# Kernel tuning notes

Measured on AMD Instinct MI355X. Metric: run time of the kernel, lower is better.

## Reference

```python
import jax, jax.numpy as jnp
import numpy as np

TAU = 1.0        # gumbel-softmax temperature
H = 8            # n_heads
RD = 32          # routing_dim


def setup_inputs() -> dict:
    key = jax.random.key(0)
    k1, k2, k3, k4, k5 = jax.random.split(key, 5)
    B, T, C = 2, 2048, 1024
    x = jax.random.normal(k1, (B, T, C), dtype=jnp.float32)
    # base adjacency [H,T,T]; keep diagonal free so each causal row has a finite logit
    base_mask = jax.random.randint(k2, (H, T, T), 0, 2).astype(bool)
    base_mask = base_mask & ~jnp.eye(T, dtype=bool)[None]
    # pre-sampled standard Gumbel noise (matches F.gumbel_softmax internals)
    u = jax.random.uniform(k3, (B, H, T, T), dtype=jnp.float32, minval=1e-9, maxval=1.0)
    gumbel = -jnp.log(-jnp.log(u))
    scale = 1.0 / np.sqrt(C).astype(np.float32)
    Wq = jax.random.normal(k4, (C, H * RD), dtype=jnp.float32) * scale
    Wk = jax.random.normal(k5, (C, H * RD), dtype=jnp.float32) * scale
    return {"x": x, "base_mask": base_mask, "gumbel": gumbel, "Wq": Wq, "Wk": Wk}


def reference(x, base_mask, gumbel, Wq, Wk):
    B, T, C = x.shape
    # routing projections -> [B,T,H,RD]
    sq = (x @ Wq).reshape(B, T, H, RD)
    sk = (x @ Wk).reshape(B, T, H, RD)
    # pairwise edge scores [B,H,T,T]
    scores = jnp.einsum("bihd,bjhd->bhij", sq, sk) / np.sqrt(RD).astype(np.float32)
    # causal mask (j > i) OR already-connected base edges -> -inf
    causal = jnp.triu(jnp.ones((T, T), dtype=bool), 1)
    mask = causal[None, None] | base_mask[None]
    scores = jnp.where(mask, -jnp.inf, scores)
    # gumbel-softmax (training path, hard=False): softmax((logits + g) / tau)
    return jax.nn.softmax((scores + gumbel) / TAU, axis=-1)
```

## Files before the change

kernel.cpp:

```cpp
#include <hip/hip_runtime.h>
#include <hip/hip_bf16.h>
#include <math.h>

#define TT    2048
#define HH    8
#define RDIM  32
#define BB    2

typedef float  f4  __attribute__((ext_vector_type(4)));
typedef int    i4  __attribute__((ext_vector_type(4)));
typedef uint   u2  __attribute__((ext_vector_type(2)));
typedef uint   u4  __attribute__((ext_vector_type(4)));
typedef short  s8v __attribute__((ext_vector_type(8)));

__device__ __forceinline__ uint rnd16(float x) {
    return (__float_as_uint(x) + 0x8000u) >> 16;
}

union v8cast { u4 u; s8v s; };

__global__ __launch_bounds__(256) void wt_prep(
    const float* __restrict__ Wq,
    const float* __restrict__ Wk,
    ushort* __restrict__ Wt)
{
    __shared__ float T[64][68];
    const int k0 = blockIdx.x * 64;
    const int n0 = blockIdx.y * 64;
    const float* W = (n0 < 256) ? Wq : Wk;
    const int nloc = n0 & 255;
    const int tid = threadIdx.x;

    #pragma unroll
    for (int r = 0; r < 4; ++r) {
        int kl  = (tid >> 4) + r * 16;
        int nl4 = (tid & 15) * 4;
        f4 v = *(const f4*)&W[(size_t)(k0 + kl) * 256 + nloc + nl4];
        T[nl4 + 0][kl] = v.x;
        T[nl4 + 1][kl] = v.y;
        T[nl4 + 2][kl] = v.z;
        T[nl4 + 3][kl] = v.w;
    }
    __syncthreads();

    const int nl = tid >> 2;
    const int kq = (tid & 3) * 16;
    u4 o0, o1;
    #pragma unroll
    for (int j = 0; j < 4; ++j) {
        uint lo = rnd16(T[nl][kq + 2 * j]);
        uint hi = rnd16(T[nl][kq + 2 * j + 1]);
        ((uint*)&o0)[j] = (hi << 16) | lo;
    }
    #pragma unroll
    for (int j = 0; j < 4; ++j) {
        uint lo = rnd16(T[nl][kq + 8 + 2 * j]);
        uint hi = rnd16(T[nl][kq + 8 + 2 * j + 1]);
        ((uint*)&o1)[j] = (hi << 16) | lo;
    }
    ushort* dst = Wt + (size_t)(n0 + nl) * 1024 + k0 + kq;
    *(u4*)dst = o0;
    *(u4*)(dst + 8) = o1;
}

__global__ __launch_bounds__(256) void proj_mfma(
    const float* __restrict__ x,
    const ushort* __restrict__ Wt,
    ushort* __restrict__ sqb,
    ushort* __restrict__ skb)
{
    const int tid = threadIdx.x;
    const int l   = tid & 63;
    const int w   = __builtin_amdgcn_readfirstlane(tid) >> 6;
    const int cl  = l & 15;
    const int g4  = l >> 4;
    const int m0  = (blockIdx.x * 4 + w) * 16;
    const int n0  = blockIdx.y * 64;

    f4 acc0 = {0,0,0,0}, acc1 = {0,0,0,0}, acc2 = {0,0,0,0}, acc3 = {0,0,0,0};

    const float*  xrow = x + (size_t)(m0 + cl) * 1024;
    const ushort* wbase = Wt + (size_t)(n0 + cl) * 1024;

    for (int ks = 0; ks < 32; ++ks) {
        const int k = ks * 32 + g4 * 8;
        f4 xa = *(const f4*)&xrow[k];
        f4 xb2 = *(const f4*)&xrow[k + 4];
        v8cast bf;
        ((uint*)&bf.u)[0] = (rnd16(xa.y) << 16) | rnd16(xa.x);
        ((uint*)&bf.u)[1] = (rnd16(xa.w) << 16) | rnd16(xa.z);
        ((uint*)&bf.u)[2] = (rnd16(xb2.y) << 16) | rnd16(xb2.x);
        ((uint*)&bf.u)[3] = (rnd16(xb2.w) << 16) | rnd16(xb2.z);
        s8v a0 = *(const s8v*)(wbase + 0 * 16 * 1024 + k);
        s8v a1 = *(const s8v*)(wbase + 1 * 16 * 1024 + k);
        s8v a2 = *(const s8v*)(wbase + 2 * 16 * 1024 + k);
        s8v a3 = *(const s8v*)(wbase + 3 * 16 * 1024 + k);
        acc0 = __builtin_amdgcn_mfma_f32_16x16x32_bf16(a0, bf.s, acc0, 0, 0, 0);
        acc1 = __builtin_amdgcn_mfma_f32_16x16x32_bf16(a1, bf.s, acc1, 0, 0, 0);
        acc2 = __builtin_amdgcn_mfma_f32_16x16x32_bf16(a2, bf.s, acc2, 0, 0, 0);
        acc3 = __builtin_amdgcn_mfma_f32_16x16x32_bf16(a3, bf.s, acc3, 0, 0, 0);
    }

    const int m = m0 + cl;
    const int nbase = n0 + g4 * 4;
    ushort* obase = (n0 < 256) ? (sqb + (size_t)m * 256 + nbase)
                               : (skb + (size_t)m * 256 + (nbase - 256));
    f4 accs[4] = {acc0, acc1, acc2, acc3};
    #pragma unroll
    for (int t = 0; t < 4; ++t) {
        u2 pk;
        pk.x = (rnd16(accs[t][1]) << 16) | rnd16(accs[t][0]);
        pk.y = (rnd16(accs[t][3]) << 16) | rnd16(accs[t][2]);
        *(u2*)(obase + t * 16) = pk;
    }
}

__global__ __launch_bounds__(512) void score_mfma(
    const ushort* __restrict__ sqb,
    const ushort* __restrict__ skb,
    const float*  __restrict__ gumbel,
    const int*    __restrict__ mask,
    float* __restrict__ out)
{
    const int tid = threadIdx.x;
    const int l   = tid & 63;
    const int w   = __builtin_amdgcn_readfirstlane(tid) >> 6;
    const int bh  = blockIdx.x & 15;
    const int sp  = blockIdx.x >> 4;
    const int h   = bh & (HH - 1);
    const int b   = bh >> 3;
    const int cl  = l & 15;
    const int g4  = l >> 4;
    const float RS = 0.17677669529663687f;

    __shared__ float sums_lds[8][16];

    const ushort* sqbase = sqb + ((size_t)b * TT) * 256 + h * RDIM + g4 * 8;
    const ushort* skbase = skb + ((size_t)b * TT) * 256 + h * RDIM + g4 * 8;
    const float*  gb = gumbel + (size_t)bh * TT * TT;
    const int*    mb = mask + (size_t)h * TT * TT;
    float*        ob = out + (size_t)bh * TT * TT;

    #pragma unroll 1
    for (int half = 0; half < 2; ++half) {
        const int s      = half ? (127 - sp) : sp;
        const int i0     = s * 16;
        const int ntiles = s + 1;
        const int zstart = ntiles * 16;
        const int i      = i0 + cl;

        s8v bfrag = *(const s8v*)(sqbase + (size_t)i * 256);

        const float* grow = gb + (size_t)i * TT;
        const int*   mrow = mb + (size_t)i * TT;
        float*       orow = ob + (size_t)i * TT;

        float sum = 0.f;
        u2 p[8][2];
        #pragma unroll
        for (int it = 0; it < 8; ++it) {
            const int jt0 = 2 * w + it * 16;
            #pragma unroll
            for (int u = 0; u < 2; ++u) {
                const int jt = jt0 + u;
                if (jt < ntiles) {
                    s8v afrag = *(const s8v*)(skbase + (size_t)(jt * 16 + cl) * 256);
                    f4 z = {0.f, 0.f, 0.f, 0.f};
                    f4 c = __builtin_amdgcn_mfma_f32_16x16x32_bf16(
                               afrag, bfrag, z, 0, 0, 0);
                    const int jb = jt * 16 + g4 * 4;
                    f4 gv = *(const f4*)&grow[jb];
                    i4 mv = *(const i4*)&mrow[jb];
                    float e0 = (jb + 0 > i || mv.x) ? 0.f : __expf(fmaf(c[0], RS, gv.x));
                    float e1 = (jb + 1 > i || mv.y) ? 0.f : __expf(fmaf(c[1], RS, gv.y));
                    float e2 = (jb + 2 > i || mv.z) ? 0.f : __expf(fmaf(c[2], RS, gv.z));
                    float e3 = (jb + 3 > i || mv.w) ? 0.f : __expf(fmaf(c[3], RS, gv.w));
                    sum += (e0 + e1) + (e2 + e3);
                    p[it][u].x = (rnd16(e1) << 16) | rnd16(e0);
                    p[it][u].y = (rnd16(e3) << 16) | rnd16(e2);
                }
            }
        }

        sum += __shfl_xor(sum, 16);
        sum += __shfl_xor(sum, 32);
        if (l < 16) sums_lds[w][l] = sum;
        __syncthreads();
        float t = 0.f;
        #pragma unroll
        for (int ww = 0; ww < 8; ++ww) t += sums_lds[ww][cl];
        const float rinv = 1.0f / t;
        __syncthreads();

        #pragma unroll
        for (int it = 0; it < 8; ++it) {
            const int jt0 = 2 * w + it * 16;
            #pragma unroll
            for (int u = 0; u < 2; ++u) {
                const int jt = jt0 + u;
                if (jt < ntiles) {
                    const int jb = jt * 16 + g4 * 4;
                    f4 v;
                    v.x = __uint_as_float(p[it][u].x << 16) * rinv;
                    v.y = __uint_as_float(p[it][u].x & 0xffff0000u) * rinv;
                    v.z = __uint_as_float(p[it][u].y << 16) * rinv;
                    v.w = __uint_as_float(p[it][u].y & 0xffff0000u) * rinv;
                    *(f4*)&orow[jb] = v;
                }
            }
        }

        for (int r = 0; r < 16; ++r) {
            for (int cz = zstart + tid * 4; cz < TT; cz += 512 * 4) {
                f4 zz = {0.f, 0.f, 0.f, 0.f};
                *(f4*)&ob[(size_t)(i0 + r) * TT + cz] = zz;
            }
        }
    }
}

extern "C" void kernel_launch(void* const* d_in, const int* in_sizes, int n_in,
                              void* d_out, int out_size, void* d_ws, size_t ws_size,
                              hipStream_t stream) {
    const float* x      = (const float*)d_in[0];
    const int*   bmask  = (const int*)d_in[1];
    const float* gumbel = (const float*)d_in[2];
    const float* Wq     = (const float*)d_in[3];
    const float* Wk     = (const float*)d_in[4];
    float* out = (float*)d_out;

    ushort* sqb = (ushort*)d_ws;
    ushort* skb = sqb + (size_t)4096 * 256;
    ushort* Wt  = skb + (size_t)4096 * 256;

    wt_prep<<<dim3(16, 8), 256, 0, stream>>>(Wq, Wk, Wt);

    proj_mfma<<<dim3(64, 8), 256, 0, stream>>>(x, Wt, sqb, skb);

    score_mfma<<<1024, 512, 0, stream>>>(sqb, skb, gumbel, bmask, out);
}
```

Measured before the change: 187.8 us.

## Double-buffer score kernel loads, stage probabilities in LDS, use nontemporal gumbel/zero stores

Software-pipelines the score kernel: the K fragment, gumbel and mask loads for the next iteration are issued before the current MFMA/exp work. The packed bf16 probabilities move from a register array into a 64 KB LDS buffer, and launch bounds now request 2 blocks per CU to cut register pressure. Gumbel reads and the zero-fill stores use nontemporal hints to avoid cache pollution. The added LDS footprint may cap occupancy, and the prefetch buffers add registers.

```diff
diff --git a/kernel.cpp b/kernel.cpp
--- a/kernel.cpp
+++ b/kernel.cpp
@@ -115,7 +115,7 @@
     }
 }
 
-__global__ __launch_bounds__(512) void score_mfma(
+__global__ __launch_bounds__(512, 2) void score_mfma(
     const ushort* __restrict__ sqb,
     const ushort* __restrict__ skb,
     const float*  __restrict__ gumbel,
@@ -133,6 +133,7 @@
     const int g4  = l >> 4;
     const float RS = 0.17677669529663687f;
 
+    __shared__ u2    p_lds[8][16][64];
     __shared__ float sums_lds[8][16];
 
     const ushort* sqbase = sqb + ((size_t)b * TT) * 256 + h * RDIM + g4 * 8;
@@ -155,32 +156,55 @@
         const int*   mrow = mb + (size_t)i * TT;
         float*       orow = ob + (size_t)i * TT;
 
+        s8v af[2][2];
+        f4  gv[2][2];
+        i4  mv[2][2];
+
+        #define PLOAD(buf_, it_) do {                                          \
+            _Pragma("unroll")                                                  \
+            for (int u_ = 0; u_ < 2; ++u_) {                                   \
+                const int jt_ = 2 * w + (it_) * 16 + u_;                       \
+                if (jt_ < ntiles) {                                            \
+                    af[buf_][u_] = *(const s8v*)(skbase +                      \
+                                     (size_t)(jt_ * 16 + cl) * 256);           \
+                    const int jb_ = jt_ * 16 + g4 * 4;                         \
+                    gv[buf_][u_] = __builtin_nontemporal_load(                 \
+                                     (const f4*)&grow[jb_]);                   \
+                    mv[buf_][u_] = *(const i4*)&mrow[jb_];                     \
+                }                                                              \
+            }                                                                  \
+        } while (0)
+
+        PLOAD(0, 0);
+
         float sum = 0.f;
-        u2 p[8][2];
         #pragma unroll
         for (int it = 0; it < 8; ++it) {
-            const int jt0 = 2 * w + it * 16;
+            const int pb = it & 1;
+            if (it < 7) PLOAD(pb ^ 1, it + 1);
             #pragma unroll
             for (int u = 0; u < 2; ++u) {
-                const int jt = jt0 + u;
+                const int jt = 2 * w + it * 16 + u;
                 if (jt < ntiles) {
-                    s8v afrag = *(const s8v*)(skbase + (size_t)(jt * 16 + cl) * 256);
                     f4 z = {0.f, 0.f, 0.f, 0.f};
                     f4 c = __builtin_amdgcn_mfma_f32_16x16x32_bf16(
-                               afrag, bfrag, z, 0, 0, 0);
+                               af[pb][u], bfrag, z, 0, 0, 0);
                     const int jb = jt * 16 + g4 * 4;
-                    f4 gv = *(const f4*)&grow[jb];
-                    i4 mv = *(const i4*)&mrow[jb];
-                    float e0 = (jb + 0 > i || mv.x) ? 0.f : __expf(fmaf(c[0], RS, gv.x));
-                    float e1 = (jb + 1 > i || mv.y) ? 0.f : __expf(fmaf(c[1], RS, gv.y));
-                    float e2 = (jb + 2 > i || mv.z) ? 0.f : __expf(fmaf(c[2], RS, gv.z));
-                    float e3 = (jb + 3 > i || mv.w) ? 0.f : __expf(fmaf(c[3], RS, gv.w));
+                    f4 gvv = gv[pb][u];
+                    i4 mvv = mv[pb][u];
+                    float e0 = (jb + 0 > i || mvv.x) ? 0.f : __expf(fmaf(c[0], RS, gvv.x));
+                    float e1 = (jb + 1 > i || mvv.y) ? 0.f : __expf(fmaf(c[1], RS, gvv.y));
+                    float e2 = (jb + 2 > i || mvv.z) ? 0.f : __expf(fmaf(c[2], RS, gvv.z));
+                    float e3 = (jb + 3 > i || mvv.w) ? 0.f : __expf(fmaf(c[3], RS, gvv.w));
                     sum += (e0 + e1) + (e2 + e3);
-                    p[it][u].x = (rnd16(e1) << 16) | rnd16(e0);
-                    p[it][u].y = (rnd16(e3) << 16) | rnd16(e2);
+                    u2 pk;
+                    pk.x = (rnd16(e1) << 16) | rnd16(e0);
+                    pk.y = (rnd16(e3) << 16) | rnd16(e2);
+                    p_lds[w][it * 2 + u][l] = pk;
                 }
             }
         }
+        #undef PLOAD
 
         sum += __shfl_xor(sum, 16);
         sum += __shfl_xor(sum, 32);
@@ -193,27 +217,24 @@
         __syncthreads();
 
         #pragma unroll
-        for (int it = 0; it < 8; ++it) {
-            const int jt0 = 2 * w + it * 16;
-            #pragma unroll
-            for (int u = 0; u < 2; ++u) {
-                const int jt = jt0 + u;
-                if (jt < ntiles) {
-                    const int jb = jt * 16 + g4 * 4;
-                    f4 v;
-                    v.x = __uint_as_float(p[it][u].x << 16) * rinv;
-                    v.y = __uint_as_float(p[it][u].x & 0xffff0000u) * rinv;
-                    v.z = __uint_as_float(p[it][u].y << 16) * rinv;
-                    v.w = __uint_as_float(p[it][u].y & 0xffff0000u) * rinv;
-                    *(f4*)&orow[jb] = v;
-                }
+        for (int sx = 0; sx < 16; ++sx) {
+            const int jt = 2 * w + (sx >> 1) * 16 + (sx & 1);
+            if (jt < ntiles) {
+                const int jb = jt * 16 + g4 * 4;
+                u2 pk = p_lds[w][sx][l];
+                f4 v;
+                v.x = __uint_as_float(pk.x << 16) * rinv;
+                v.y = __uint_as_float(pk.x & 0xffff0000u) * rinv;
+                v.z = __uint_as_float(pk.y << 16) * rinv;
+                v.w = __uint_as_float(pk.y & 0xffff0000u) * rinv;
+                *(f4*)&orow[jb] = v;
             }
         }
 
         for (int r = 0; r < 16; ++r) {
             for (int cz = zstart + tid * 4; cz < TT; cz += 512 * 4) {
                 f4 zz = {0.f, 0.f, 0.f, 0.f};
-                *(f4*)&ob[(size_t)(i0 + r) * TT + cz] = zz;
+                __builtin_nontemporal_store(zz, (f4*)&ob[(size_t)(i0 + r) * TT + cz]);
             }
         }
     }
@@ -234,7 +255,6 @@
     ushort* Wt  = skb + (size_t)4096 * 256;
 
     wt_prep<<<dim3(16, 8), 256, 0, stream>>>(Wq, Wk, Wt);
-
     proj_mfma<<<dim3(64, 8), 256, 0, stream>>>(x, Wt, sqb, skb);
 
     score_mfma<<<1024, 512, 0, stream>>>(sqb, skb, gumbel, bmask, out);
```

New measurement: 197.6 us, median of 3. 5.2% more time.

## Software-pipeline score kernel loads and stage probabilities in LDS across halves

Applied to the files above, without the earlier changes.

Restructures the score kernel into a 3-deep register pipeline that issues key fragment, gumbel and mask loads two groups ahead of the MFMA/exp compute. The packed bf16 probabilities move from registers to LDS so more waves can stay resident, and launch bounds request 2 blocks per CU. The second half's first loads are issued before the first half's normalise/write pass so that latency is hidden. The zero fill also switches to nontemporal stores. It adds 64KB of LDS per block and double-buffers the reduction sums, which may limit occupancy.

```diff
diff --git a/kernel.cpp b/kernel.cpp
--- a/kernel.cpp
+++ b/kernel.cpp
@@ -115,7 +115,7 @@
     }
 }
 
-__global__ __launch_bounds__(512) void score_mfma(
+__global__ __launch_bounds__(512, 2) void score_mfma(
     const ushort* __restrict__ sqb,
     const ushort* __restrict__ skb,
     const float*  __restrict__ gumbel,
@@ -133,7 +133,8 @@
     const int g4  = l >> 4;
     const float RS = 0.17677669529663687f;
 
-    __shared__ float sums_lds[8][16];
+    __shared__ u2    p_lds[8][16][64];
+    __shared__ float sums_lds[2][8][16];
 
     const ushort* sqbase = sqb + ((size_t)b * TT) * 256 + h * RDIM + g4 * 8;
     const ushort* skbase = skb + ((size_t)b * TT) * 256 + h * RDIM + g4 * 8;
@@ -141,82 +142,151 @@
     const int*    mb = mask + (size_t)h * TT * TT;
     float*        ob = out + (size_t)bh * TT * TT;
 
-    #pragma unroll 1
-    for (int half = 0; half < 2; ++half) {
-        const int s      = half ? (127 - sp) : sp;
-        const int i0     = s * 16;
-        const int ntiles = s + 1;
-        const int zstart = ntiles * 16;
-        const int i      = i0 + cl;
-
-        s8v bfrag = *(const s8v*)(sqbase + (size_t)i * 256);
-
-        const float* grow = gb + (size_t)i * TT;
-        const int*   mrow = mb + (size_t)i * TT;
-        float*       orow = ob + (size_t)i * TT;
-
-        float sum = 0.f;
-        u2 p[8][2];
-        #pragma unroll
-        for (int it = 0; it < 8; ++it) {
-            const int jt0 = 2 * w + it * 16;
-            #pragma unroll
-            for (int u = 0; u < 2; ++u) {
-                const int jt = jt0 + u;
-                if (jt < ntiles) {
-                    s8v afrag = *(const s8v*)(skbase + (size_t)(jt * 16 + cl) * 256);
-                    f4 z = {0.f, 0.f, 0.f, 0.f};
-                    f4 c = __builtin_amdgcn_mfma_f32_16x16x32_bf16(
-                               afrag, bfrag, z, 0, 0, 0);
-                    const int jb = jt * 16 + g4 * 4;
-                    f4 gv = *(const f4*)&grow[jb];
-                    i4 mv = *(const i4*)&mrow[jb];
-                    float e0 = (jb + 0 > i || mv.x) ? 0.f : __expf(fmaf(c[0], RS, gv.x));
-                    float e1 = (jb + 1 > i || mv.y) ? 0.f : __expf(fmaf(c[1], RS, gv.y));
-                    float e2 = (jb + 2 > i || mv.z) ? 0.f : __expf(fmaf(c[2], RS, gv.z));
-                    float e3 = (jb + 3 > i || mv.w) ? 0.f : __expf(fmaf(c[3], RS, gv.w));
-                    sum += (e0 + e1) + (e2 + e3);
-                    p[it][u].x = (rnd16(e1) << 16) | rnd16(e0);
-                    p[it][u].y = (rnd16(e3) << 16) | rnd16(e2);
-                }
-            }
-        }
-
-        sum += __shfl_xor(sum, 16);
-        sum += __shfl_xor(sum, 32);
-        if (l < 16) sums_lds[w][l] = sum;
-        __syncthreads();
-        float t = 0.f;
-        #pragma unroll
-        for (int ww = 0; ww < 8; ++ww) t += sums_lds[ww][cl];
-        const float rinv = 1.0f / t;
-        __syncthreads();
-
-        #pragma unroll
-        for (int it = 0; it < 8; ++it) {
-            const int jt0 = 2 * w + it * 16;
-            #pragma unroll
-            for (int u = 0; u < 2; ++u) {
-                const int jt = jt0 + u;
-                if (jt < ntiles) {
-                    const int jb = jt * 16 + g4 * 4;
-                    f4 v;
-                    v.x = __uint_as_float(p[it][u].x << 16) * rinv;
-                    v.y = __uint_as_float(p[it][u].x & 0xffff0000u) * rinv;
-                    v.z = __uint_as_float(p[it][u].y << 16) * rinv;
-                    v.w = __uint_as_float(p[it][u].y & 0xffff0000u) * rinv;
-                    *(f4*)&orow[jb] = v;
-                }
-            }
-        }
-
-        for (int r = 0; r < 16; ++r) {
-            for (int cz = zstart + tid * 4; cz < TT; cz += 512 * 4) {
-                f4 zz = {0.f, 0.f, 0.f, 0.f};
-                *(f4*)&ob[(size_t)(i0 + r) * TT + cz] = zz;
-            }
-        }
-    }
+    const int s0_ = sp,        s1_ = 127 - sp;
+    const int i00 = s0_ * 16,  i01 = s1_ * 16;
+    const int nt0 = s0_ + 1,   nt1 = s1_ + 1;
+    const int i_0 = i00 + cl,  i_1 = i01 + cl;
+    const float* grow0 = gb + (size_t)i_0 * TT;
+    const float* grow1 = gb + (size_t)i_1 * TT;
+    const int*   mrow0 = mb + (size_t)i_0 * TT;
+    const int*   mrow1 = mb + (size_t)i_1 * TT;
+    float*       orow0 = ob + (size_t)i_0 * TT;
+    float*       orow1 = ob + (size_t)i_1 * TT;
+
+    s8v bf0 = *(const s8v*)(sqbase + (size_t)i_0 * 256);
+    s8v bf1 = *(const s8v*)(sqbase + (size_t)i_1 * 256);
+
+    s8v af[3][2];
+    f4  gv[3][2];
+    i4  mv[3][2];
+
+    #define PLOAD(gp_) do {                                                   \
+        const int buf_ = (gp_) % 3;                                           \
+        const int pr_  = (gp_) & 7;                                           \
+        const bool hh_ = (gp_) >= 8;                                          \
+        const int nt_  = hh_ ? nt1 : nt0;                                     \
+        const float* g_ = hh_ ? grow1 : grow0;                                \
+        const int*   m_ = hh_ ? mrow1 : mrow0;                                \
+        _Pragma("unroll")                                                     \
+        for (int u_ = 0; u_ < 2; ++u_) {                                      \
+            const int jt_ = 2 * w + pr_ * 16 + u_;                            \
+            if (jt_ < nt_) {                                                  \
+                af[buf_][u_] = *(const s8v*)(skbase +                         \
+                                 (size_t)(jt_ * 16 + cl) * 256);              \
+                const int jb_ = jt_ * 16 + g4 * 4;                            \
+                gv[buf_][u_] = *(const f4*)&g_[jb_];                          \
+                mv[buf_][u_] = *(const i4*)&m_[jb_];                          \
+            }                                                                 \
+        }                                                                     \
+    } while (0)
+
+    #define PCOMPUTE(gp_, sum_) do {                                          \
+        const int buf_ = (gp_) % 3;                                           \
+        const int pr_  = (gp_) & 7;                                           \
+        const bool hh_ = (gp_) >= 8;                                          \
+        const int nt_  = hh_ ? nt1 : nt0;                                     \
+        const int iw_  = hh_ ? i_1 : i_0;                                     \
+        const s8v bfr_ = hh_ ? bf1 : bf0;                                     \
+        _Pragma("unroll")                                                     \
+        for (int u_ = 0; u_ < 2; ++u_) {                                      \
+            const int jt_ = 2 * w + pr_ * 16 + u_;                            \
+            if (jt_ < nt_) {                                                  \
+                f4 z_ = {0.f, 0.f, 0.f, 0.f};                                 \
+                f4 c_ = __builtin_amdgcn_mfma_f32_16x16x32_bf16(              \
+                            af[buf_][u_], bfr_, z_, 0, 0, 0);                 \
+                const int jb_ = jt_ * 16 + g4 * 4;                            \
+                f4 gvv_ = gv[buf_][u_];                                       \
+                i4 mvv_ = mv[buf_][u_];                                       \
+                float e0_ = (jb_ + 0 > iw_ || mvv_.x) ? 0.f : __expf(fmaf(c_[0], RS, gvv_.x)); \
+                float e1_ = (jb_ + 1 > iw_ || mvv_.y) ? 0.f : __expf(fmaf(c_[1], RS, gvv_.y)); \
+                float e2_ = (jb_ + 2 > iw_ || mvv_.z) ? 0.f : __expf(fmaf(c_[2], RS, gvv_.z)); \
+                float e3_ = (jb_ + 3 > iw_ || mvv_.w) ? 0.f : __expf(fmaf(c_[3], RS, gvv_.w)); \
+                sum_ += (e0_ + e1_) + (e2_ + e3_);                            \
+                u2 pk_;                                                       \
+                pk_.x = (rnd16(e1_) << 16) | rnd16(e0_);                      \
+                pk_.y = (rnd16(e3_) << 16) | rnd16(e2_);                      \
+                p_lds[w][pr_ * 2 + u_][l] = pk_;                              \
+            }                                                                 \
+        }                                                                     \
+    } while (0)
+
+    #define REDUCE(hbuf_, sum_, rinv_) do {                                   \
+        float v_ = sum_;                                                      \
+        v_ += __shfl_xor(v_, 16);                                             \
+        v_ += __shfl_xor(v_, 32);                                             \
+        if (l < 16) sums_lds[hbuf_][w][l] = v_;                               \
+        __syncthreads();                                                      \
+        float t_ = 0.f;                                                       \
+        _Pragma("unroll")                                                     \
+        for (int ww_ = 0; ww_ < 8; ++ww_) t_ += sums_lds[hbuf_][ww_][cl];     \
+        rinv_ = 1.0f / t_;                                                    \
+    } while (0)
+
+    #define PASS2(rinv_, nt_, orow_) do {                                     \
+        _Pragma("unroll")                                                     \
+        for (int sx_ = 0; sx_ < 16; ++sx_) {                                  \
+            const int jt_ = 2 * w + (sx_ >> 1) * 16 + (sx_ & 1);              \
+            if (jt_ < nt_) {                                                  \
+                const int jb_ = jt_ * 16 + g4 * 4;                            \
+                u2 pk_ = p_lds[w][sx_][l];                                    \
+                f4 v_;                                                        \
+                v_.x = __uint_as_float(pk_.x << 16) * rinv_;                  \
+                v_.y = __uint_as_float(pk_.x & 0xffff0000u) * rinv_;          \
+                v_.z = __uint_as_float(pk_.y << 16) * rinv_;                  \
+                v_.w = __uint_as_float(pk_.y & 0xffff0000u) * rinv_;          \
+                *(f4*)&orow_[jb_] = v_;                                       \
+            }                                                                 \
+        }                                                                     \
+    } while (0)
+
+    #define ZFILL(i0_, nt_) do {                                              \
+        const int zs_ = (nt_) * 16;                                           \
+        for (int r_ = 0; r_ < 16; ++r_) {                                     \
+            for (int cz_ = zs_ + tid * 4; cz_ < TT; cz_ += 512 * 4) {         \
+                f4 zz_ = {0.f, 0.f, 0.f, 0.f};                                \
+                __builtin_nontemporal_store(zz_,                              \
+                    (f4*)&ob[(size_t)((i0_) + r_) * TT + cz_]);               \
+            }                                                                 \
+        }                                                                     \
+    } while (0)
+
+    PLOAD(0);
+    PLOAD(1);
+
+    float sum0 = 0.f;
+    #pragma unroll
+    for (int gp = 0; gp < 8; ++gp) {
+        if (gp + 2 < 8) PLOAD(gp + 2);
+        PCOMPUTE(gp, sum0);
+    }
+
+    float rinv0;
+    REDUCE(0, sum0, rinv0);
+
+    PLOAD(8);
+    PLOAD(9);
+
+    PASS2(rinv0, nt0, orow0);
+    ZFILL(i00, nt0);
+
+    float sum1 = 0.f;
+    #pragma unroll
+    for (int gp = 8; gp < 16; ++gp) {
+        if (gp + 2 < 16) PLOAD(gp + 2);
+        PCOMPUTE(gp, sum1);
+    }
+
+    float rinv1;
+    REDUCE(1, sum1, rinv1);
+
+    PASS2(rinv1, nt1, orow1);
+    ZFILL(i01, nt1);
+
+    #undef PLOAD
+    #undef PCOMPUTE
+    #undef REDUCE
+    #undef PASS2
+    #undef ZFILL
 }
 
 extern "C" void kernel_launch(void* const* d_in, const int* in_sizes, int n_in,
@@ -234,7 +304,6 @@
     ushort* Wt  = skb + (size_t)4096 * 256;
 
     wt_prep<<<dim3(16, 8), 256, 0, stream>>>(Wq, Wk, Wt);
-
     proj_mfma<<<dim3(64, 8), 256, 0, stream>>>(x, Wt, sqb, skb);
 
     score_mfma<<<1024, 512, 0, stream>>>(sqb, skb, gumbel, bmask, out);
```

After: 196.5 us. 1.05x slower.

## Move upper-triangle zero fill from score kernel into projection kernel

Applied to the files above, without the earlier changes.

Writing zeros to the causally masked upper triangle of the output moves out of the score kernel and into the projection kernel, which has 512 blocks each zeroing four row-strips. This shrinks the score kernel to only the lower-triangle work and its output writes. Per-half LDS buffers for the row sums let the second barrier be removed. The projection kernel now carries about half the output bandwidth, which adds to its runtime and may not overlap with anything, since the two kernels run in sequence on the same stream.

```diff
diff --git a/kernel.cpp b/kernel.cpp
--- a/kernel.cpp
+++ b/kernel.cpp
@@ -67,7 +67,8 @@
     const float* __restrict__ x,
     const ushort* __restrict__ Wt,
     ushort* __restrict__ sqb,
-    ushort* __restrict__ skb)
+    ushort* __restrict__ skb,
+    float* __restrict__ out)
 {
     const int tid = threadIdx.x;
     const int l   = tid & 63;
@@ -113,6 +114,27 @@
         pk.y = (rnd16(accs[t][3]) << 16) | rnd16(accs[t][2]);
         *(u2*)(obase + t * 16) = pk;
     }
+
+    {
+        const int zb  = blockIdx.y * 64 + blockIdx.x;
+        const int zbh = zb & 15;
+        const int sp2 = zb >> 4;
+        float* ob = out + (size_t)zbh * TT * TT;
+        const int ss[4] = {sp2, 63 - sp2, 64 + sp2, 127 - sp2};
+        #pragma unroll
+        for (int q = 0; q < 4; ++q) {
+            const int s  = ss[q];
+            const int i0 = s * 16;
+            const int zs = (s + 1) * 16;
+            for (int r = 0; r < 16; ++r) {
+                float* row = &ob[(size_t)(i0 + r) * TT];
+                for (int cz = zs + tid * 4; cz < TT; cz += 256 * 4) {
+                    f4 zz = {0.f, 0.f, 0.f, 0.f};
+                    *(f4*)&row[cz] = zz;
+                }
+            }
+        }
+    }
 }
 
 __global__ __launch_bounds__(512) void score_mfma(
@@ -133,7 +155,7 @@
     const int g4  = l >> 4;
     const float RS = 0.17677669529663687f;
 
-    __shared__ float sums_lds[8][16];
+    __shared__ float sums_lds[2][8][16];
 
     const ushort* sqbase = sqb + ((size_t)b * TT) * 256 + h * RDIM + g4 * 8;
     const ushort* skbase = skb + ((size_t)b * TT) * 256 + h * RDIM + g4 * 8;
@@ -146,7 +168,6 @@
         const int s      = half ? (127 - sp) : sp;
         const int i0     = s * 16;
         const int ntiles = s + 1;
-        const int zstart = ntiles * 16;
         const int i      = i0 + cl;
 
         s8v bfrag = *(const s8v*)(sqbase + (size_t)i * 256);
@@ -184,13 +205,12 @@
 
         sum += __shfl_xor(sum, 16);
         sum += __shfl_xor(sum, 32);
-        if (l < 16) sums_lds[w][l] = sum;
+        if (l < 16) sums_lds[half][w][l] = sum;
         __syncthreads();
         float t = 0.f;
         #pragma unroll
-        for (int ww = 0; ww < 8; ++ww) t += sums_lds[ww][cl];
+        for (int ww = 0; ww < 8; ++ww) t += sums_lds[half][ww][cl];
         const float rinv = 1.0f / t;
-        __syncthreads();
 
         #pragma unroll
         for (int it = 0; it < 8; ++it) {
@@ -209,13 +229,6 @@
                 }
             }
         }
-
-        for (int r = 0; r < 16; ++r) {
-            for (int cz = zstart + tid * 4; cz < TT; cz += 512 * 4) {
-                f4 zz = {0.f, 0.f, 0.f, 0.f};
-                *(f4*)&ob[(size_t)(i0 + r) * TT + cz] = zz;
-            }
-        }
     }
 }
 
@@ -235,7 +248,7 @@
 
     wt_prep<<<dim3(16, 8), 256, 0, stream>>>(Wq, Wk, Wt);
 
-    proj_mfma<<<dim3(64, 8), 256, 0, stream>>>(x, Wt, sqb, skb);
+    proj_mfma<<<dim3(64, 8), 256, 0, stream>>>(x, Wt, sqb, skb, out);
 
     score_mfma<<<1024, 512, 0, stream>>>(sqb, skb, gumbel, bmask, out);
 }
```

Result: faster. 184.1 us (median of 2 runs) (-2.0%).
